# Performance work log

Measured on AMD Instinct MI355X. Metric: run time of the kernel, lower is better.

## Reference

```python
import jax, jax.numpy as jnp
import numpy as np

HIDDEN = 512
HEADS = 8
HEAD_DIM = HIDDEN // HEADS


def setup_inputs() -> dict:
    key = jax.random.key(0)
    ks = jax.random.split(key, 12)
    B, S = 2, 2048
    s = 1.0 / np.sqrt(HIDDEN)
    inp = {
        "query": jax.random.normal(ks[0], (B, S, HIDDEN), dtype=jnp.float32),
        "key": jax.random.normal(ks[1], (B, S, HIDDEN), dtype=jnp.float32),
        "value": jax.random.normal(ks[2], (B, S, HIDDEN), dtype=jnp.float32),
        "Wq": jax.random.uniform(ks[3], (HIDDEN, HIDDEN), jnp.float32, -s, s),
        "bq": jnp.zeros((HIDDEN,), jnp.float32),
        "Wk": jax.random.uniform(ks[4], (HIDDEN, HIDDEN), jnp.float32, -s, s),
        "bk": jnp.zeros((HIDDEN,), jnp.float32),
        "Wv": jax.random.uniform(ks[5], (HIDDEN, HIDDEN), jnp.float32, -s, s),
        "bv": jnp.zeros((HIDDEN,), jnp.float32),
        "Wo": jax.random.uniform(ks[6], (HIDDEN, HIDDEN), jnp.float32, -s, s),
        "bo": jnp.zeros((HIDDEN,), jnp.float32),
    }
    return inp


def reference(query, key, value, Wq, bq, Wk, bk, Wv, bv, Wo, bo):
    B, S, _ = query.shape
    scale = jnp.sqrt(jnp.asarray(HEAD_DIM, dtype=query.dtype))
    # Linear projections (torch Linear: x @ W.T + b)
    Q = (query @ Wq.T + bq).reshape(B, S, HEADS, HEAD_DIM).transpose(0, 2, 1, 3)
    K = (key @ Wk.T + bk).reshape(B, S, HEADS, HEAD_DIM).transpose(0, 2, 1, 3)
    V = (value @ Wv.T + bv).reshape(B, S, HEADS, HEAD_DIM).transpose(0, 2, 1, 3)
    # Scores: [B, H, S, S]
    energy = jnp.einsum("bhqd,bhkd->bhqk", Q, K) / scale
    attn = jax.nn.softmax(energy, axis=-1)
    # Dropout is identity in eval mode.
    x = jnp.einsum("bhqk,bhkd->bhqd", attn, V)
    x = x.transpose(0, 2, 1, 3).reshape(B, S, HIDDEN)
    return x @ Wo.T + bo
```

## Files before the change

kernel.cpp:

```cpp
#include <hip/hip_runtime.h>

typedef __bf16 bf16x8 __attribute__((ext_vector_type(8)));
typedef float f32x4 __attribute__((ext_vector_type(4)));
typedef unsigned int uint4v __attribute__((ext_vector_type(4)));
typedef unsigned int uint2v __attribute__((ext_vector_type(2)));

__device__ __forceinline__ unsigned short f2bf(float f) {
  union { float f; unsigned int u; } v; v.f = f;
  unsigned int u = v.u;
  u += 0x7FFFu + ((u >> 16) & 1u);
  return (unsigned short)(u >> 16);
}

__device__ __forceinline__ unsigned int pack2bf(float a, float b) {
  return (unsigned int)f2bf(a) | ((unsigned int)f2bf(b) << 16);
}

__global__ __launch_bounds__(256) void convert_w(
    const float* wq, const float* wk, const float* wv, const float* wo,
    unsigned short* wqc, unsigned short* wkc, unsigned short* wvc,
    unsigned short* woc, float qscale)
{
  const float* src; unsigned short* dst; float sc = 1.f;
  switch (blockIdx.y) {
    case 0: src = wq; dst = wqc; sc = qscale; break;
    case 1: src = wk; dst = wkc; break;
    case 2: src = wv; dst = wvc; break;
    default: src = wo; dst = woc; break;
  }
  int idx = (blockIdx.x * 256 + threadIdx.x) * 8;
  f32x4 a = *(const f32x4*)(src + idx);
  f32x4 b = *(const f32x4*)(src + idx + 4);
  uint4v p;
  p.x = pack2bf(a.x * sc, a.y * sc);
  p.y = pack2bf(a.z * sc, a.w * sc);
  p.z = pack2bf(b.x * sc, b.y * sc);
  p.w = pack2bf(b.z * sc, b.w * sc);
  *(uint4v*)(dst + idx) = p;
}

template<int OUT, bool AF32>
__device__ __forceinline__ void gemm_core(
    const void* __restrict__ Ap, const unsigned short* __restrict__ W,
    const float* __restrict__ bias, void* __restrict__ Cp,
    float bscale, int mbase, int nbase)
{
  __shared__ union {
    struct { unsigned short As[64][40]; unsigned short Bs[128][40]; } t;
    unsigned short Cs[128][72];
  } u;

  const int tid  = threadIdx.x;
  const int wave = tid >> 6, lane = tid & 63;
  const int lrow = lane & 15, lgrp = lane >> 4;
  const int ar = tid >> 2, ac = (tid & 3) * 8;

  const unsigned short* Bg0 = W + (size_t)(nbase + ar) * 512 + ac;
  const unsigned short* Bg1 = W + (size_t)(nbase + ar + 64) * 512 + ac;

  f32x4 acc[4][2];
#pragma unroll
  for (int i = 0; i < 4; i++)
#pragma unroll
    for (int j = 0; j < 2; j++) acc[i][j] = (f32x4){0.f, 0.f, 0.f, 0.f};

  const unsigned short* Ab = (const unsigned short*)Ap;
  const float*          Af = (const float*)Ap;
  uint4v pA; f32x4 pAf0, pAf1;
  if constexpr (AF32) {
    const float* base = Af + (size_t)(mbase + ar) * 512 + ac;
    pAf0 = *(const f32x4*)(base);
    pAf1 = *(const f32x4*)(base + 4);
  } else {
    pA = *(const uint4v*)(Ab + (size_t)(mbase + ar) * 512 + ac);
  }
  uint4v pB0 = *(const uint4v*)Bg0;
  uint4v pB1 = *(const uint4v*)Bg1;

  for (int kt = 0; kt < 512; kt += 32) {
    __syncthreads();
    if constexpr (AF32) {
      uint4v w;
      w.x = pack2bf(pAf0.x, pAf0.y); w.y = pack2bf(pAf0.z, pAf0.w);
      w.z = pack2bf(pAf1.x, pAf1.y); w.w = pack2bf(pAf1.z, pAf1.w);
      *(uint4v*)&u.t.As[ar][ac] = w;
    } else {
      *(uint4v*)&u.t.As[ar][ac] = pA;
    }
    *(uint4v*)&u.t.Bs[ar][ac]      = pB0;
    *(uint4v*)&u.t.Bs[ar + 64][ac] = pB1;
    __syncthreads();
    if (kt + 32 < 512) {
      if constexpr (AF32) {
        const float* base = Af + (size_t)(mbase + ar) * 512 + ac + kt + 32;
        pAf0 = *(const f32x4*)(base);
        pAf1 = *(const f32x4*)(base + 4);
      } else {
        pA = *(const uint4v*)(Ab + (size_t)(mbase + ar) * 512 + ac + kt + 32);
      }
      pB0 = *(const uint4v*)(Bg0 + kt + 32);
      pB1 = *(const uint4v*)(Bg1 + kt + 32);
    }
    bf16x8 a[4], b[2];
#pragma unroll
    for (int mi = 0; mi < 4; mi++)
      a[mi] = *(const bf16x8*)&u.t.As[mi * 16 + lrow][lgrp * 8];
#pragma unroll
    for (int ni = 0; ni < 2; ni++)
      b[ni] = *(const bf16x8*)&u.t.Bs[wave * 32 + ni * 16 + lrow][lgrp * 8];
#pragma unroll
    for (int mi = 0; mi < 4; mi++)
#pragma unroll
      for (int ni = 0; ni < 2; ni++)
        acc[mi][ni] = __builtin_amdgcn_mfma_f32_16x16x32_bf16(
            a[mi], b[ni], acc[mi][ni], 0, 0, 0);
  }

  if constexpr (OUT == 2) {
    __syncthreads();
#pragma unroll
    for (int ni = 0; ni < 2; ni++) {
      int col_l = wave * 32 + ni * 16 + lrow;
      float bv = bias[nbase + col_l];
#pragma unroll
      for (int mi = 0; mi < 4; mi++) {
        int row_l = mi * 16 + lgrp * 4;
#pragma unroll
        for (int r = 0; r < 4; r++)
          u.Cs[col_l][row_l + r] = f2bf(acc[mi][ni][r] + bv);
      }
    }
    __syncthreads();
    const int bb = mbase >> 11, s_base = mbase & 2047;
    unsigned short* Vt = (unsigned short*)Cp;
#pragma unroll
    for (int ks = 0; ks < 4; ks++) {
      int seg = tid + ks * 256;
      int c = seg >> 3, r0 = (seg & 7) * 8;
      uint4v val = *(const uint4v*)&u.Cs[c][r0];
      int n = nbase + c, hh = n >> 6, d = n & 63;
      *(uint4v*)(Vt + ((size_t)(bb * 8 + hh) * 64 + d) * 2048 + s_base + r0) = val;
    }
  } else {
#pragma unroll
    for (int ni = 0; ni < 2; ni++) {
      int col = nbase + wave * 32 + ni * 16 + lrow;
      float bv = bias[col] * bscale;
#pragma unroll
      for (int mi = 0; mi < 4; mi++) {
        int row0 = mbase + mi * 16 + lgrp * 4;
#pragma unroll
        for (int r = 0; r < 4; r++) {
          float val = acc[mi][ni][r] + bv;
          if constexpr (OUT == 0)
            ((unsigned short*)Cp)[(size_t)(row0 + r) * 512 + col] = f2bf(val);
          else
            ((float*)Cp)[(size_t)(row0 + r) * 512 + col] = val;
        }
      }
    }
  }
}

__global__ __launch_bounds__(256) void qkv_gemm(
    const float* q, const float* k, const float* v,
    const unsigned short* wqc, const unsigned short* wkc,
    const unsigned short* wvc,
    const float* bq, const float* bk, const float* bv,
    unsigned short* Qb, unsigned short* Kb, unsigned short* Vt, float qscale)
{
  const int z = blockIdx.z;
  const int mb = blockIdx.y * 64, nb = blockIdx.x * 128;
  if (z == 2)      gemm_core<2, true>(v, wvc, bv, Vt, 1.f, mb, nb);
  else if (z == 0) gemm_core<0, true>(q, wqc, bq, Qb, qscale, mb, nb);
  else             gemm_core<0, true>(k, wkc, bk, Kb, 1.f, mb, nb);
}

__global__ __launch_bounds__(256) void out_gemm(
    const unsigned short* ctx, const unsigned short* woc,
    const float* bo, float* out)
{
  gemm_core<1, false>(ctx, woc, bo, out, 1.f, blockIdx.y * 64, blockIdx.x * 128);
}

__global__ __launch_bounds__(256) void attn_kernel(
    const unsigned short* Qb, const unsigned short* Kb,
    const unsigned short* Vt, unsigned short* ctx)
{
  __shared__ unsigned short Ks[128][74];
  __shared__ unsigned short Vs[64][140];
  __shared__ unsigned short Ps[2][64][76];

  const int tid  = threadIdx.x;
  const int wave = tid >> 6, lane = tid & 63;
  const int lrow = lane & 15, lgrp = lane >> 4;
  const int qh = wave >> 1, kh = wave & 1;
  const int bh = blockIdx.y, b = bh >> 3, h = bh & 7;
  const int qbase = blockIdx.x * 64;

  const unsigned short* Qg  = Qb + (size_t)(b * 2048 + qbase) * 512 + h * 64;
  const unsigned short* Kg  = Kb + (size_t)(b * 2048) * 512 + h * 64;
  const unsigned short* Vtg = Vt + (size_t)bh * 64 * 2048;

#pragma unroll
  for (int i = 0; i < 2; i++) {
    int seg = tid + i * 256;
    int row = seg >> 3, c0 = (seg & 7) * 8;
    *(uint4v*)&Ps[0][row][c0] = *(const uint4v*)(Qg + (size_t)row * 512 + c0);
  }
  __syncthreads();
  bf16x8 qf[2][2];
#pragma unroll
  for (int mi = 0; mi < 2; mi++)
#pragma unroll
    for (int c = 0; c < 2; c++)
      qf[mi][c] = *(const bf16x8*)&Ps[0][qh * 32 + mi * 16 + lrow][c * 32 + lgrp * 8];

  const int s0 = tid >> 3, kc_ = (tid & 7) * 8;
  const int krow0 = ((s0 & 15) << 3) | (s0 >> 4);
  const int vd_ = tid >> 4, vcl = (tid & 15);

  float lst[2][4] = {{0.f,0.f,0.f,0.f},{0.f,0.f,0.f,0.f}};
  f32x4 oacc[2][4];
#pragma unroll
  for (int mi = 0; mi < 2; mi++)
#pragma unroll
    for (int d = 0; d < 4; d++) oacc[mi][d] = (f32x4){0.f, 0.f, 0.f, 0.f};

  uint4v kr[4], vr[4];
#pragma unroll
  for (int i = 0; i < 4; i++) {
    kr[i] = *(const uint4v*)(Kg + (size_t)(krow0 + 2 * i) * 512 + kc_);
    vr[i] = *(const uint4v*)(Vtg + (size_t)(vd_ + 16 * i) * 2048 + vcl * 8);
  }

  for (int it = 0; it < 16; ++it) {
    __syncthreads();
#pragma unroll
    for (int i = 0; i < 4; i++) {
      *(uint4v*)&Ks[s0 + 32 * i][kc_] = kr[i];
      *(uint2v*)&Vs[vd_ + 16 * i][vcl * 4]      = (uint2v){vr[i].x, vr[i].y};
      *(uint2v*)&Vs[vd_ + 16 * i][64 + vcl * 4] = (uint2v){vr[i].z, vr[i].w};
    }
    __syncthreads();
    if (it < 15) {
      const int key0 = (it + 1) * 128;
#pragma unroll
      for (int i = 0; i < 4; i++) {
        kr[i] = *(const uint4v*)(Kg + (size_t)(key0 + krow0 + 2 * i) * 512 + kc_);
        vr[i] = *(const uint4v*)(Vtg + (size_t)(vd_ + 16 * i) * 2048 + key0 + vcl * 8);
      }
    }

    f32x4 sacc[2][4];
#pragma unroll
    for (int mi = 0; mi < 2; mi++)
#pragma unroll
      for (int ni = 0; ni < 4; ni++) sacc[mi][ni] = (f32x4){0.f, 0.f, 0.f, 0.f};
#pragma unroll
    for (int ni = 0; ni < 4; ni++) {
      const int t = 4 * kh + ni;
      bf16x8 k0 = *(const bf16x8*)&Ks[t * 16 + lrow][lgrp * 8];
      bf16x8 k1 = *(const bf16x8*)&Ks[t * 16 + lrow][32 + lgrp * 8];
#pragma unroll
      for (int mi = 0; mi < 2; mi++) {
        sacc[mi][ni] = __builtin_amdgcn_mfma_f32_16x16x32_bf16(qf[mi][0], k0, sacc[mi][ni], 0, 0, 0);
        sacc[mi][ni] = __builtin_amdgcn_mfma_f32_16x16x32_bf16(qf[mi][1], k1, sacc[mi][ni], 0, 0, 0);
      }
    }

#pragma unroll
    for (int mi = 0; mi < 2; mi++)
#pragma unroll
      for (int ni = 0; ni < 4; ni++)
#pragma unroll
        for (int r = 0; r < 4; r++) {
          float p = exp2f(sacc[mi][ni][r]);
          sacc[mi][ni][r] = p;
          lst[mi][r] += p;
        }

#pragma unroll
    for (int mi = 0; mi < 2; mi++)
#pragma unroll
      for (int r = 0; r < 4; r++) {
        uint2v pk;
        pk.x = pack2bf(sacc[mi][0][r], sacc[mi][1][r]);
        pk.y = pack2bf(sacc[mi][2][r], sacc[mi][3][r]);
        *(uint2v*)&Ps[kh][qh * 32 + mi * 16 + lgrp * 4 + r][lrow * 4] = pk;
      }

#pragma unroll
    for (int ks = 0; ks < 2; ks++) {
      bf16x8 pa[2];
#pragma unroll
      for (int mi = 0; mi < 2; mi++)
        pa[mi] = *(const bf16x8*)&Ps[kh][qh * 32 + mi * 16 + lrow][ks * 32 + lgrp * 8];
#pragma unroll
      for (int dt = 0; dt < 4; dt++) {
        bf16x8 vb = *(const bf16x8*)&Vs[dt * 16 + lrow][kh * 64 + ks * 32 + lgrp * 8];
#pragma unroll
        for (int mi = 0; mi < 2; mi++)
          oacc[mi][dt] = __builtin_amdgcn_mfma_f32_16x16x32_bf16(pa[mi], vb, oacc[mi][dt], 0, 0, 0);
      }
    }
  }

#pragma unroll
  for (int m = 1; m < 16; m <<= 1)
#pragma unroll
    for (int mi = 0; mi < 2; mi++)
#pragma unroll
      for (int r = 0; r < 4; r++) lst[mi][r] += __shfl_xor(lst[mi][r], m, 64);

  __syncthreads();
  float* Obuf = (float*)&Ks[0][0];
  float* Lbuf = (float*)&Vs[0][0];
  if (kh == 1) {
#pragma unroll
    for (int mi = 0; mi < 2; mi++)
#pragma unroll
      for (int r = 0; r < 4; r++) {
        int row = qh * 32 + mi * 16 + lgrp * 4 + r;
#pragma unroll
        for (int dt = 0; dt < 4; dt++)
          Obuf[row * 68 + dt * 16 + lrow] = oacc[mi][dt][r];
        if (lrow == 0) Lbuf[row] = lst[mi][r];
      }
  }
  __syncthreads();
  if (kh == 0) {
    unsigned short* Cg = ctx + (size_t)(b * 2048 + qbase) * 512 + h * 64;
#pragma unroll
    for (int mi = 0; mi < 2; mi++)
#pragma unroll
      for (int r = 0; r < 4; r++) {
        int row = qh * 32 + mi * 16 + lgrp * 4 + r;
        float inv = 1.0f / (lst[mi][r] + Lbuf[row]);
#pragma unroll
        for (int dt = 0; dt < 4; dt++) {
          float val = (oacc[mi][dt][r] + Obuf[row * 68 + dt * 16 + lrow]) * inv;
          Cg[(size_t)(qbase >= 0 ? row : row) * 512 + dt * 16 + lrow] = f2bf(val);
        }
      }
  }
}

extern "C" void kernel_launch(void* const* d_in, const int* in_sizes, int n_in,
                              void* d_out, int out_size, void* d_ws, size_t ws_size,
                              hipStream_t stream)
{
  const float* q  = (const float*)d_in[0];
  const float* k  = (const float*)d_in[1];
  const float* v  = (const float*)d_in[2];
  const float* Wq = (const float*)d_in[3];
  const float* bq = (const float*)d_in[4];
  const float* Wk = (const float*)d_in[5];
  const float* bk = (const float*)d_in[6];
  const float* Wv = (const float*)d_in[7];
  const float* bv = (const float*)d_in[8];
  const float* Wo = (const float*)d_in[9];
  const float* bo = (const float*)d_in[10];
  float* out = (float*)d_out;

  unsigned short* wqc = (unsigned short*)d_ws;
  unsigned short* wkc = wqc + (1 << 18);
  unsigned short* wvc = wkc + (1 << 18);
  unsigned short* woc = wvc + (1 << 18);
  unsigned short* Qb  = woc + (1 << 18);
  unsigned short* Kb  = Qb  + (1 << 21);
  unsigned short* Vt  = Kb  + (1 << 21);
  unsigned short* Cb  = Vt  + (1 << 21);

  const float qscale = 0.125f * 1.44269504088896340736f;

  convert_w<<<dim3(128, 4), 256, 0, stream>>>(
      Wq, Wk, Wv, Wo, wqc, wkc, wvc, woc, qscale);
  qkv_gemm<<<dim3(4, 64, 3), 256, 0, stream>>>(
      q, k, v, wqc, wkc, wvc, bq, bk, bv, Qb, Kb, Vt, qscale);
  attn_kernel<<<dim3(32, 16), 256, 0, stream>>>(Qb, Kb, Vt, Cb);
  out_gemm<<<dim3(4, 64), 256, 0, stream>>>(Cb, woc, bo, out);
}
```

Baseline: 159.8 us.

## Pre-convert activations to bf16, drop LDS staging in GEMM, fold row-sum into MFMA

Activations q/k/v are converted to bf16 in a separate pass alongside the weights. The GEMM core then loads MFMA operands straight from global memory into registers, with no shared-memory staging and no barriers. In attention, the softmax denominator is computed by an extra MFMA against a row of ones appended to V, replacing the per-element sum and the shuffle reductions. The kernel also uses the hardware exp2 and truncating bf16 packing. This trades an extra global round trip for the activations, uncoalesced per-lane global loads and slightly lower precision for fewer barriers and fewer VALU ops.

```diff
diff --git a/kernel.cpp b/kernel.cpp
--- a/kernel.cpp
+++ b/kernel.cpp
@@ -16,19 +16,34 @@
   return (unsigned int)f2bf(a) | ((unsigned int)f2bf(b) << 16);
 }
 
-__global__ __launch_bounds__(256) void convert_w(
+__device__ __forceinline__ unsigned int packtrunc(float a, float b) {
+  return __builtin_amdgcn_perm(__float_as_uint(b), __float_as_uint(a),
+                               0x07060302u);
+}
+
+__device__ __forceinline__ bf16x8 as_bf(uint4v u) {
+  union { uint4v u; bf16x8 b; } c; c.u = u; return c.b;
+}
+
+__global__ __launch_bounds__(256) void convert_kernel(
+    const float* q, const float* k, const float* v,
     const float* wq, const float* wk, const float* wv, const float* wo,
+    unsigned short* qc, unsigned short* kc, unsigned short* vc,
     unsigned short* wqc, unsigned short* wkc, unsigned short* wvc,
     unsigned short* woc, float qscale)
 {
-  const float* src; unsigned short* dst; float sc = 1.f;
+  const float* src; unsigned short* dst; int n; float sc = 1.f;
   switch (blockIdx.y) {
-    case 0: src = wq; dst = wqc; sc = qscale; break;
-    case 1: src = wk; dst = wkc; break;
-    case 2: src = wv; dst = wvc; break;
-    default: src = wo; dst = woc; break;
+    case 0: src = q;  dst = qc;  n = 1 << 21; break;
+    case 1: src = k;  dst = kc;  n = 1 << 21; break;
+    case 2: src = v;  dst = vc;  n = 1 << 21; break;
+    case 3: src = wq; dst = wqc; n = 1 << 18; sc = qscale; break;
+    case 4: src = wk; dst = wkc; n = 1 << 18; break;
+    case 5: src = wv; dst = wvc; n = 1 << 18; break;
+    default: src = wo; dst = woc; n = 1 << 18; break;
   }
   int idx = (blockIdx.x * 256 + threadIdx.x) * 8;
+  if (idx >= n) return;
   f32x4 a = *(const f32x4*)(src + idx);
   f32x4 b = *(const f32x4*)(src + idx + 4);
   uint4v p;
@@ -39,24 +54,26 @@
   *(uint4v*)(dst + idx) = p;
 }
 
-template<int OUT, bool AF32>
+template<int OUT>
 __device__ __forceinline__ void gemm_core(
-    const void* __restrict__ Ap, const unsigned short* __restrict__ W,
+    const unsigned short* __restrict__ A, const unsigned short* __restrict__ W,
     const float* __restrict__ bias, void* __restrict__ Cp,
     float bscale, int mbase, int nbase)
 {
-  __shared__ union {
-    struct { unsigned short As[64][40]; unsigned short Bs[128][40]; } t;
-    unsigned short Cs[128][72];
-  } u;
+  __shared__ unsigned short Cs[128][72];
 
   const int tid  = threadIdx.x;
   const int wave = tid >> 6, lane = tid & 63;
   const int lrow = lane & 15, lgrp = lane >> 4;
-  const int ar = tid >> 2, ac = (tid & 3) * 8;
-
-  const unsigned short* Bg0 = W + (size_t)(nbase + ar) * 512 + ac;
-  const unsigned short* Bg1 = W + (size_t)(nbase + ar + 64) * 512 + ac;
+
+  const unsigned short* Ap[4];
+  const unsigned short* Wp[2];
+#pragma unroll
+  for (int mi = 0; mi < 4; mi++)
+    Ap[mi] = A + (size_t)(mbase + mi * 16 + lrow) * 512 + lgrp * 8;
+#pragma unroll
+  for (int ni = 0; ni < 2; ni++)
+    Wp[ni] = W + (size_t)(nbase + wave * 32 + ni * 16 + lrow) * 512 + lgrp * 8;
 
   f32x4 acc[4][2];
 #pragma unroll
@@ -64,60 +81,32 @@
 #pragma unroll
     for (int j = 0; j < 2; j++) acc[i][j] = (f32x4){0.f, 0.f, 0.f, 0.f};
 
-  const unsigned short* Ab = (const unsigned short*)Ap;
-  const float*          Af = (const float*)Ap;
-  uint4v pA; f32x4 pAf0, pAf1;
-  if constexpr (AF32) {
-    const float* base = Af + (size_t)(mbase + ar) * 512 + ac;
-    pAf0 = *(const f32x4*)(base);
-    pAf1 = *(const f32x4*)(base + 4);
-  } else {
-    pA = *(const uint4v*)(Ab + (size_t)(mbase + ar) * 512 + ac);
-  }
-  uint4v pB0 = *(const uint4v*)Bg0;
-  uint4v pB1 = *(const uint4v*)Bg1;
+  uint4v ca[4], cb[2], na[4], nb[2];
+#pragma unroll
+  for (int mi = 0; mi < 4; mi++) ca[mi] = *(const uint4v*)(Ap[mi]);
+#pragma unroll
+  for (int ni = 0; ni < 2; ni++) cb[ni] = *(const uint4v*)(Wp[ni]);
 
   for (int kt = 0; kt < 512; kt += 32) {
-    __syncthreads();
-    if constexpr (AF32) {
-      uint4v w;
-      w.x = pack2bf(pAf0.x, pAf0.y); w.y = pack2bf(pAf0.z, pAf0.w);
-      w.z = pack2bf(pAf1.x, pAf1.y); w.w = pack2bf(pAf1.z, pAf1.w);
-      *(uint4v*)&u.t.As[ar][ac] = w;
-    } else {
-      *(uint4v*)&u.t.As[ar][ac] = pA;
-    }
-    *(uint4v*)&u.t.Bs[ar][ac]      = pB0;
-    *(uint4v*)&u.t.Bs[ar + 64][ac] = pB1;
-    __syncthreads();
     if (kt + 32 < 512) {
-      if constexpr (AF32) {
-        const float* base = Af + (size_t)(mbase + ar) * 512 + ac + kt + 32;
-        pAf0 = *(const f32x4*)(base);
-        pAf1 = *(const f32x4*)(base + 4);
-      } else {
-        pA = *(const uint4v*)(Ab + (size_t)(mbase + ar) * 512 + ac + kt + 32);
-      }
-      pB0 = *(const uint4v*)(Bg0 + kt + 32);
-      pB1 = *(const uint4v*)(Bg1 + kt + 32);
-    }
-    bf16x8 a[4], b[2];
-#pragma unroll
-    for (int mi = 0; mi < 4; mi++)
-      a[mi] = *(const bf16x8*)&u.t.As[mi * 16 + lrow][lgrp * 8];
-#pragma unroll
-    for (int ni = 0; ni < 2; ni++)
-      b[ni] = *(const bf16x8*)&u.t.Bs[wave * 32 + ni * 16 + lrow][lgrp * 8];
+#pragma unroll
+      for (int mi = 0; mi < 4; mi++) na[mi] = *(const uint4v*)(Ap[mi] + kt + 32);
+#pragma unroll
+      for (int ni = 0; ni < 2; ni++) nb[ni] = *(const uint4v*)(Wp[ni] + kt + 32);
+    }
 #pragma unroll
     for (int mi = 0; mi < 4; mi++)
 #pragma unroll
       for (int ni = 0; ni < 2; ni++)
         acc[mi][ni] = __builtin_amdgcn_mfma_f32_16x16x32_bf16(
-            a[mi], b[ni], acc[mi][ni], 0, 0, 0);
+            as_bf(ca[mi]), as_bf(cb[ni]), acc[mi][ni], 0, 0, 0);
+#pragma unroll
+    for (int mi = 0; mi < 4; mi++) ca[mi] = na[mi];
+#pragma unroll
+    for (int ni = 0; ni < 2; ni++) cb[ni] = nb[ni];
   }
 
   if constexpr (OUT == 2) {
-    __syncthreads();
 #pragma unroll
     for (int ni = 0; ni < 2; ni++) {
       int col_l = wave * 32 + ni * 16 + lrow;
@@ -127,7 +116,7 @@
         int row_l = mi * 16 + lgrp * 4;
 #pragma unroll
         for (int r = 0; r < 4; r++)
-          u.Cs[col_l][row_l + r] = f2bf(acc[mi][ni][r] + bv);
+          Cs[col_l][row_l + r] = f2bf(acc[mi][ni][r] + bv);
       }
     }
     __syncthreads();
@@ -137,7 +126,7 @@
     for (int ks = 0; ks < 4; ks++) {
       int seg = tid + ks * 256;
       int c = seg >> 3, r0 = (seg & 7) * 8;
-      uint4v val = *(const uint4v*)&u.Cs[c][r0];
+      uint4v val = *(const uint4v*)&Cs[c][r0];
       int n = nbase + c, hh = n >> 6, d = n & 63;
       *(uint4v*)(Vt + ((size_t)(bb * 8 + hh) * 64 + d) * 2048 + s_base + r0) = val;
     }
@@ -163,7 +152,7 @@
 }
 
 __global__ __launch_bounds__(256) void qkv_gemm(
-    const float* q, const float* k, const float* v,
+    const unsigned short* qc, const unsigned short* kc, const unsigned short* vc,
     const unsigned short* wqc, const unsigned short* wkc,
     const unsigned short* wvc,
     const float* bq, const float* bk, const float* bv,
@@ -171,16 +160,16 @@
 {
   const int z = blockIdx.z;
   const int mb = blockIdx.y * 64, nb = blockIdx.x * 128;
-  if (z == 2)      gemm_core<2, true>(v, wvc, bv, Vt, 1.f, mb, nb);
-  else if (z == 0) gemm_core<0, true>(q, wqc, bq, Qb, qscale, mb, nb);
-  else             gemm_core<0, true>(k, wkc, bk, Kb, 1.f, mb, nb);
+  if (z == 2)      gemm_core<2>(vc, wvc, bv, Vt, 1.f, mb, nb);
+  else if (z == 0) gemm_core<0>(qc, wqc, bq, Qb, qscale, mb, nb);
+  else             gemm_core<0>(kc, wkc, bk, Kb, 1.f, mb, nb);
 }
 
 __global__ __launch_bounds__(256) void out_gemm(
     const unsigned short* ctx, const unsigned short* woc,
     const float* bo, float* out)
 {
-  gemm_core<1, false>(ctx, woc, bo, out, 1.f, blockIdx.y * 64, blockIdx.x * 128);
+  gemm_core<1>(ctx, woc, bo, out, 1.f, blockIdx.y * 64, blockIdx.x * 128);
 }
 
 __global__ __launch_bounds__(256) void attn_kernel(
@@ -188,7 +177,7 @@
     const unsigned short* Vt, unsigned short* ctx)
 {
   __shared__ unsigned short Ks[128][74];
-  __shared__ unsigned short Vs[64][140];
+  __shared__ unsigned short Vs[80][140];
   __shared__ unsigned short Ps[2][64][76];
 
   const int tid  = threadIdx.x;
@@ -208,6 +197,11 @@
     int row = seg >> 3, c0 = (seg & 7) * 8;
     *(uint4v*)&Ps[0][row][c0] = *(const uint4v*)(Qg + (size_t)row * 512 + c0);
   }
+  {
+    int row = 64 + (tid >> 4), c0 = (tid & 15) * 8;
+    unsigned int one2 = 0x3F803F80u;
+    *(uint4v*)&Vs[row][c0] = (uint4v){one2, one2, one2, one2};
+  }
   __syncthreads();
   bf16x8 qf[2][2];
 #pragma unroll
@@ -220,12 +214,11 @@
   const int krow0 = ((s0 & 15) << 3) | (s0 >> 4);
   const int vd_ = tid >> 4, vcl = (tid & 15);
 
-  float lst[2][4] = {{0.f,0.f,0.f,0.f},{0.f,0.f,0.f,0.f}};
-  f32x4 oacc[2][4];
+  f32x4 oacc[2][5];
 #pragma unroll
   for (int mi = 0; mi < 2; mi++)
 #pragma unroll
-    for (int d = 0; d < 4; d++) oacc[mi][d] = (f32x4){0.f, 0.f, 0.f, 0.f};
+    for (int d = 0; d < 5; d++) oacc[mi][d] = (f32x4){0.f, 0.f, 0.f, 0.f};
 
   uint4v kr[4], vr[4];
 #pragma unroll
@@ -274,19 +267,15 @@
 #pragma unroll
       for (int ni = 0; ni < 4; ni++)
 #pragma unroll
-        for (int r = 0; r < 4; r++) {
-          float p = exp2f(sacc[mi][ni][r]);
-          sacc[mi][ni][r] = p;
-          lst[mi][r] += p;
-        }
-
+        for (int r = 0; r < 4; r++)
+          sacc[mi][ni][r] = __builtin_amdgcn_exp2f(sacc[mi][ni][r]);
 #pragma unroll
     for (int mi = 0; mi < 2; mi++)
 #pragma unroll
       for (int r = 0; r < 4; r++) {
         uint2v pk;
-        pk.x = pack2bf(sacc[mi][0][r], sacc[mi][1][r]);
-        pk.y = pack2bf(sacc[mi][2][r], sacc[mi][3][r]);
+        pk.x = packtrunc(sacc[mi][0][r], sacc[mi][1][r]);
+        pk.y = packtrunc(sacc[mi][2][r], sacc[mi][3][r]);
         *(uint2v*)&Ps[kh][qh * 32 + mi * 16 + lgrp * 4 + r][lrow * 4] = pk;
       }
 
@@ -297,7 +286,7 @@
       for (int mi = 0; mi < 2; mi++)
         pa[mi] = *(const bf16x8*)&Ps[kh][qh * 32 + mi * 16 + lrow][ks * 32 + lgrp * 8];
 #pragma unroll
-      for (int dt = 0; dt < 4; dt++) {
+      for (int dt = 0; dt < 5; dt++) {
         bf16x8 vb = *(const bf16x8*)&Vs[dt * 16 + lrow][kh * 64 + ks * 32 + lgrp * 8];
 #pragma unroll
         for (int mi = 0; mi < 2; mi++)
@@ -305,13 +294,6 @@
       }
     }
   }
-
-#pragma unroll
-  for (int m = 1; m < 16; m <<= 1)
-#pragma unroll
-    for (int mi = 0; mi < 2; mi++)
-#pragma unroll
-      for (int r = 0; r < 4; r++) lst[mi][r] += __shfl_xor(lst[mi][r], m, 64);
 
   __syncthreads();
   float* Obuf = (float*)&Ks[0][0];
@@ -325,7 +307,7 @@
 #pragma unroll
         for (int dt = 0; dt < 4; dt++)
           Obuf[row * 68 + dt * 16 + lrow] = oacc[mi][dt][r];
-        if (lrow == 0) Lbuf[row] = lst[mi][r];
+        if (lrow == 0) Lbuf[row] = oacc[mi][4][r];
       }
   }
   __syncthreads();
@@ -336,11 +318,11 @@
 #pragma unroll
       for (int r = 0; r < 4; r++) {
         int row = qh * 32 + mi * 16 + lgrp * 4 + r;
-        float inv = 1.0f / (lst[mi][r] + Lbuf[row]);
+        float inv = 1.0f / (oacc[mi][4][r] + Lbuf[row]);
 #pragma unroll
         for (int dt = 0; dt < 4; dt++) {
           float val = (oacc[mi][dt][r] + Obuf[row * 68 + dt * 16 + lrow]) * inv;
-          Cg[(size_t)(qbase >= 0 ? row : row) * 512 + dt * 16 + lrow] = f2bf(val);
+          Cg[(size_t)row * 512 + dt * 16 + lrow] = f2bf(val);
         }
       }
   }
@@ -363,21 +345,24 @@
   const float* bo = (const float*)d_in[10];
   float* out = (float*)d_out;
 
-  unsigned short* wqc = (unsigned short*)d_ws;
+  unsigned short* qc  = (unsigned short*)d_ws;
+  unsigned short* kc  = qc  + (size_t)1 * (1 << 21);
+  unsigned short* vc  = qc  + (size_t)2 * (1 << 21);
+  unsigned short* wqc = qc  + (size_t)3 * (1 << 21);
   unsigned short* wkc = wqc + (1 << 18);
   unsigned short* wvc = wkc + (1 << 18);
   unsigned short* woc = wvc + (1 << 18);
   unsigned short* Qb  = woc + (1 << 18);
   unsigned short* Kb  = Qb  + (1 << 21);
   unsigned short* Vt  = Kb  + (1 << 21);
-  unsigned short* Cb  = Vt  + (1 << 21);
+  unsigned short* Cb  = qc;
 
   const float qscale = 0.125f * 1.44269504088896340736f;
 
-  convert_w<<<dim3(128, 4), 256, 0, stream>>>(
-      Wq, Wk, Wv, Wo, wqc, wkc, wvc, woc, qscale);
+  convert_kernel<<<dim3(1024, 7), 256, 0, stream>>>(
+      q, k, v, Wq, Wk, Wv, Wo, qc, kc, vc, wqc, wkc, wvc, woc, qscale);
   qkv_gemm<<<dim3(4, 64, 3), 256, 0, stream>>>(
-      q, k, v, wqc, wkc, wvc, bq, bk, bv, Qb, Kb, Vt, qscale);
+      qc, kc, vc, wqc, wkc, wvc, bq, bk, bv, Qb, Kb, Vt, qscale);
   attn_kernel<<<dim3(32, 16), 256, 0, stream>>>(Qb, Kb, Vt, Cb);
   out_gemm<<<dim3(4, 64), 256, 0, stream>>>(Cb, woc, bo, out);
 }
```

Measured after the change: 179.7 us. 1.13x slower.
